# Optimization experiments

Hardware: AMD Instinct MI355X
Metric: run time of the kernel (lower is better)

## Reference

```python
import jax, jax.numpy as jnp
import numpy as np

B, S, D = 4, 4096, 1024
GROUP = 256
HEAD = 128
INNER = 2048


def setup_inputs() -> dict:
    key = jax.random.key(0)
    ks = jax.random.split(key, 16)
    s = 0.02
    return {
        'x': jax.random.normal(ks[0], (B, S, D), jnp.float32),
        'Wv': jax.random.normal(ks[1], (D, INNER), jnp.float32) * s,
        'bv': jnp.zeros((INNER,), jnp.float32),
        'Wg': jax.random.normal(ks[2], (D, INNER), jnp.float32) * s,
        'bg': jnp.zeros((INNER,), jnp.float32),
        'Win': jax.random.normal(ks[3], (D, HEAD), jnp.float32) * s,
        'bin_': jnp.zeros((HEAD,), jnp.float32),
        'Wout': jax.random.normal(ks[4], (INNER, D), jnp.float32) * s,
        'bout': jnp.zeros((D,), jnp.float32),
        'g_qq': 1.0 + jax.random.normal(ks[5], (HEAD,), jnp.float32) * s,
        'b_qq': jnp.zeros((HEAD,), jnp.float32),
        'g_qk': 1.0 + jax.random.normal(ks[6], (HEAD,), jnp.float32) * s,
        'b_qk': jnp.zeros((HEAD,), jnp.float32),
        'g_lq': 1.0 + jax.random.normal(ks[7], (HEAD,), jnp.float32) * s,
        'b_lq': jnp.zeros((HEAD,), jnp.float32),
        'g_lk': 1.0 + jax.random.normal(ks[8], (HEAD,), jnp.float32) * s,
        'b_lk': jnp.zeros((HEAD,), jnp.float32),
    }


def reference(x, Wv, bv, Wg, bg, Win, bin_, Wout, bout,
              g_qq, b_qq, g_qk, b_qk, g_lq, b_lq, g_lk, b_lk):
    b, s, d = x.shape
    g = s // GROUP
    xc = x.reshape(b, g, GROUP, d)                       # [B,G,C,D]
    v = jax.nn.silu(xc @ Wv + bv)                        # [B,G,C,E]
    gate = jax.nn.silu(xc @ Wg + bg)                     # [B,G,C,E]
    x_ = jax.nn.silu(xc @ Win + bin_)                    # [B,G,C,H]
    quad_q = x_ * g_qq + b_qq
    quad_k = x_ * g_qk + b_qk
    lin_q = x_ * g_lq + b_lq
    lin_k = x_ * g_lk + b_lk
    # local quadratic relu^2 attention per chunk
    scale = jnp.asarray(INNER ** 0.5, x.dtype)           # v.size(-1)**0.5
    attn = jnp.einsum('bgns,bgms->bgnm', quad_q, quad_k) / scale
    causal_mask = jnp.triu(jnp.ones((GROUP, GROUP), bool), 1)
    attn = jnp.where(causal_mask, 0.0, attn)
    attn = jnp.square(jax.nn.relu(attn))
    v_quad = jnp.einsum('bgnm,bgme->bgne', attn, v)
    # global causal linear attention: exclusive cumsum of per-chunk k^T v over chunks
    kv = jnp.einsum('bgcs,bgce->bgse', lin_k, v)         # [B,G,H,E]
    kv = jnp.cumsum(kv, axis=1) - kv                     # exclusive over chunk dim
    v_lin = jnp.einsum('bgcs,bgse->bgce', lin_q, kv)
    o = (v_quad + v_lin) * gate
    o = o @ Wout + bout
    return o.reshape(b, s, d)
```

## Files before the change

kernel.cpp:

```cpp
#include <hip/hip_runtime.h>

typedef __attribute__((ext_vector_type(8))) short short8;
typedef __attribute__((ext_vector_type(4))) float floatx4;
typedef __attribute__((ext_vector_type(4))) unsigned short ushort4v;
typedef unsigned short u16;

#define DEV __device__ __forceinline__

DEV u16 f2bf(float f) {
  unsigned int u = __float_as_uint(f);
  u += 0x7fffu + ((u >> 16) & 1u);
  return (u16)(u >> 16);
}
DEV float bf2f(u16 h) { return __uint_as_float(((unsigned int)h) << 16); }
DEV float silu_f(float x) { return x / (1.f + __expf(-x)); }
DEV floatx4 fzero() { floatx4 z = {0.f, 0.f, 0.f, 0.f}; return z; }
DEV floatx4 mfma16(short8 a, short8 b, floatx4 c) {
  return __builtin_amdgcn_mfma_f32_16x16x32_bf16(a, b, c, 0, 0, 0);
}
DEV void gll16(const void* g, void* l) {
  __builtin_amdgcn_global_load_lds((__attribute__((address_space(1))) void*)g,
                                   (__attribute__((address_space(3))) void*)l,
                                   16, 0, 0);
}

__global__ __launch_bounds__(256) void cast_x_kernel(const float* __restrict__ x,
                                                     u16* __restrict__ xb, int n4) {
  int i = blockIdx.x * 256 + threadIdx.x;
  if (i >= n4) return;
  float4 v = ((const float4*)x)[i];
  ushort4v o;
  o[0] = f2bf(v.x); o[1] = f2bf(v.y); o[2] = f2bf(v.z); o[3] = f2bf(v.w);
  *(ushort4v*)&xb[(size_t)i * 4] = o;
}

__global__ __launch_bounds__(256) void transpose_cast_kernel(const float* __restrict__ W,
                                                             u16* __restrict__ WT,
                                                             int K, int N) {
  __shared__ u16 tile[32][36];
  int n0 = blockIdx.x * 32, k0 = blockIdx.y * 32;
  int t = threadIdx.x;
  int r = t >> 3, cs = (t & 7) * 4;
  float4 v = *(const float4*)&W[(size_t)(k0 + r) * N + n0 + cs];
  tile[r][cs + 0] = f2bf(v.x);
  tile[r][cs + 1] = f2bf(v.y);
  tile[r][cs + 2] = f2bf(v.z);
  tile[r][cs + 3] = f2bf(v.w);
  __syncthreads();
  ushort4v o;
  o[0] = tile[cs + 0][r];
  o[1] = tile[cs + 1][r];
  o[2] = tile[cs + 2][r];
  o[3] = tile[cs + 3][r];
  *(ushort4v*)&WT[(size_t)(n0 + r) * K + k0 + cs] = o;
}

DEV void wave_transposed_store(u16* __restrict__ Ct, long chunk_stride,
                               const u16* trw, int chunk, int cbase, int nbase,
                               int lane) {
#pragma unroll
  for (int it = 0; it < 8; ++it) {
    int e_l = it * 8 + (lane >> 3);
    int c_off = (lane & 7) * 8;
    short8 val = *(const short8*)&trw[e_l * 72 + c_off];
    *(short8*)&Ct[(size_t)chunk * chunk_stride + (size_t)(nbase + e_l) * 256 + cbase +
                  c_off] = val;
  }
}

template <int MODE>
__global__ __launch_bounds__(256) void gemm_bt(
    const u16* __restrict__ A, const u16* __restrict__ Bt, int M, int N, int K,
    const float* __restrict__ bias, u16* __restrict__ Cn, float* __restrict__ Cf,
    u16* __restrict__ Ct, long ct_stride, u16* __restrict__ Cn2, u16* __restrict__ Cn3,
    const float* __restrict__ gqq, const float* __restrict__ bqq,
    const float* __restrict__ gqk, const float* __restrict__ bqk,
    const float* __restrict__ glq, const float* __restrict__ blq,
    const float* __restrict__ glk, const float* __restrict__ blk) {
  __shared__ union {
    struct { u16 a[128 * 32]; u16 b[128 * 32]; } st;
    u16 tr[4 * 64 * 72];
  } sm;
  const int t = threadIdx.x;
  const int wave = t >> 6, lane = t & 63;
  const int l15 = lane & 15, l16 = lane >> 4;
  const int n0 = blockIdx.x * 128, m0 = blockIdx.y * 128;
  const int wm = (wave >> 1) * 64, wn = (wave & 1) * 64;

  floatx4 acc[4][4];
#pragma unroll
  for (int i = 0; i < 4; ++i)
#pragma unroll
    for (int j = 0; j < 4; ++j) acc[i][j] = fzero();

  const int c0 = t, c1 = 256 + t;
  const int r0s = c0 >> 2, p0s = c0 & 3;
  const int r1s = c1 >> 2, p1s = c1 & 3;
  const int g0 = p0s ^ ((r0s >> 1) & 3);
  const int g1 = p1s ^ ((r1s >> 1) & 3);
  const u16* pa0 = A + (size_t)(m0 + r0s) * K + g0 * 8;
  const u16* pa1 = A + (size_t)(m0 + r1s) * K + g1 * 8;
  const u16* pb0 = Bt + (size_t)(n0 + r0s) * K + g0 * 8;
  const u16* pb1 = Bt + (size_t)(n0 + r1s) * K + g1 * 8;
  const int sw = (l15 >> 1) & 3;

  for (int k0 = 0; k0 < K; k0 += 32) {
    __syncthreads();
    gll16(pa0 + k0, &sm.st.a[c0 * 8]);
    gll16(pa1 + k0, &sm.st.a[c1 * 8]);
    gll16(pb0 + k0, &sm.st.b[c0 * 8]);
    gll16(pb1 + k0, &sm.st.b[c1 * 8]);
    __syncthreads();
    short8 af[4], bfr[4];
#pragma unroll
    for (int mi = 0; mi < 4; ++mi)
      af[mi] = *(const short8*)&sm.st.a[(wm + mi * 16 + l15) * 32 + (l16 ^ sw) * 8];
#pragma unroll
    for (int ni = 0; ni < 4; ++ni)
      bfr[ni] = *(const short8*)&sm.st.b[(wn + ni * 16 + l15) * 32 + (l16 ^ sw) * 8];
#pragma unroll
    for (int mi = 0; mi < 4; ++mi)
#pragma unroll
      for (int ni = 0; ni < 4; ++ni)
        acc[mi][ni] = mfma16(af[mi], bfr[ni], acc[mi][ni]);
  }
  __syncthreads();

  if constexpr (MODE == 0) {
    u16* trw = &sm.tr[wave * 64 * 72];
#pragma unroll
    for (int mi = 0; mi < 4; ++mi)
#pragma unroll
      for (int ni = 0; ni < 4; ++ni) {
        const int col = n0 + wn + ni * 16 + l15;
        const float bc = bias[col];
#pragma unroll
        for (int r = 0; r < 4; ++r)
          trw[(mi * 16 + l16 * 4 + r) * 72 + ni * 16 + l15] =
              f2bf(silu_f(acc[mi][ni][r] + bc));
      }
#pragma unroll
    for (int it = 0; it < 8; ++it) {
      const int m_l = it * 8 + (lane >> 3);
      const int n_off = (lane & 7) * 8;
      *(short8*)&Cn[(size_t)(m0 + wm + m_l) * N + n0 + wn + n_off] =
          *(const short8*)&trw[m_l * 72 + n_off];
    }
  } else if constexpr (MODE == 3) {
#pragma unroll
    for (int mi = 0; mi < 4; ++mi)
#pragma unroll
      for (int ni = 0; ni < 4; ++ni) {
        const int col = n0 + wn + ni * 16 + l15;
        const float bc = bias[col];
        const int row = m0 + wm + mi * 16 + l16 * 4;
#pragma unroll
        for (int r = 0; r < 4; ++r)
          Cf[(size_t)(row + r) * N + col] = acc[mi][ni][r] + bc;
      }
  } else if constexpr (MODE == 1) {
    u16* trw = &sm.tr[wave * 64 * 72];
#pragma unroll
    for (int mi = 0; mi < 4; ++mi)
#pragma unroll
      for (int ni = 0; ni < 4; ++ni) {
        const int col = n0 + wn + ni * 16 + l15;
        const float bc = bias[col];
        ushort4v p;
#pragma unroll
        for (int r = 0; r < 4; ++r) p[r] = f2bf(silu_f(acc[mi][ni][r] + bc));
        *(ushort4v*)&trw[(ni * 16 + l15) * 72 + mi * 16 + l16 * 4] = p;
      }
    wave_transposed_store(Ct, ct_stride, trw, (m0 + wm) >> 8, (m0 + wm) & 255,
                          n0 + wn, lane);
  } else {
    u16* trw = &sm.tr[wave * 64 * 72];
#pragma unroll
    for (int mi = 0; mi < 4; ++mi)
#pragma unroll
      for (int ni = 0; ni < 4; ++ni) {
        const int col = wn + ni * 16 + l15;
        const float bc = bias[col];
        const float Gqq = gqq[col], Bqq = bqq[col];
        const float Gqk = gqk[col], Bqk = bqk[col];
        const float Glq = glq[col], Blq = blq[col];
        const float Glk = glk[col], Blk = blk[col];
        const int row = m0 + wm + mi * 16 + l16 * 4;
        ushort4v p;
#pragma unroll
        for (int r = 0; r < 4; ++r) {
          const float sv = silu_f(acc[mi][ni][r] + bc);
          const size_t ad = (size_t)(row + r) * N + col;
          Cn[ad] = f2bf(sv * Gqq + Bqq);
          Cn2[ad] = f2bf(sv * Gqk + Bqk);
          Cn3[ad] = f2bf(sv * Glq + Blq);
          p[r] = f2bf(sv * Glk + Blk);
        }
        *(ushort4v*)&trw[(ni * 16 + l15) * 72 + mi * 16 + l16 * 4] = p;
      }
    wave_transposed_store(Ct, ct_stride, trw, (m0 + wm) >> 8, (m0 + wm) & 255, wn,
                          lane);
  }
}

__global__ __launch_bounds__(256) void kv_kernel(const u16* __restrict__ vT,
                                                 const u16* __restrict__ lkT,
                                                 u16* __restrict__ kv) {
  const int chunk = blockIdx.y;
  const int et = blockIdx.x;
  const int w = threadIdx.x >> 6, lane = threadIdx.x & 63;
  const int l15 = lane & 15, l16 = lane >> 4;
  const size_t vb = (size_t)chunk * (2048 * 256) + (size_t)et * (128 * 256);
  const size_t lb = (size_t)chunk * (128 * 256);
  const int we = (w >> 1) * 64, wh = (w & 1) * 64;
  floatx4 acc[4][4];
#pragma unroll
  for (int i = 0; i < 4; ++i)
#pragma unroll
    for (int j = 0; j < 4; ++j) acc[i][j] = fzero();
  for (int kk = 0; kk < 8; ++kk) {
    short8 av[4], bv[4];
#pragma unroll
    for (int mi = 0; mi < 4; ++mi)
      av[mi] = *(const short8*)&vT[vb + (size_t)(we + mi * 16 + l15) * 256 + kk * 32 +
                                   l16 * 8];
#pragma unroll
    for (int ni = 0; ni < 4; ++ni)
      bv[ni] = *(const short8*)&lkT[lb + (size_t)(wh + ni * 16 + l15) * 256 + kk * 32 +
                                    l16 * 8];
#pragma unroll
    for (int mi = 0; mi < 4; ++mi)
#pragma unroll
      for (int ni = 0; ni < 4; ++ni) acc[mi][ni] = mfma16(av[mi], bv[ni], acc[mi][ni]);
  }
  u16* out = kv + (size_t)chunk * (2048 * 128);
#pragma unroll
  for (int mi = 0; mi < 4; ++mi)
#pragma unroll
    for (int ni = 0; ni < 4; ++ni) {
      const int h = wh + ni * 16 + l15;
      const int e = et * 128 + we + mi * 16 + l16 * 4;
#pragma unroll
      for (int r = 0; r < 4; ++r) out[(size_t)(e + r) * 128 + h] = f2bf(acc[mi][ni][r]);
    }
}

__global__ __launch_bounds__(256) void cumsum_kernel(u16* __restrict__ kv) {
  const int idx = blockIdx.x * 256 + threadIdx.x;
  const int b = blockIdx.y;
  float s = 0.f;
  for (int g = 0; g < 16; ++g) {
    const size_t a = (size_t)(b * 16 + g) * 262144 + idx;
    const float v = bf2f(kv[a]);
    kv[a] = f2bf(s);
    s += v;
  }
}

__global__ __launch_bounds__(256) void attn_kernel(
    const u16* __restrict__ qq, const u16* __restrict__ qk, const u16* __restrict__ lq,
    const u16* __restrict__ vT, const u16* __restrict__ kvT,
    u16* __restrict__ gate_op) {
  __shared__ u16 S[64][264];
  const int chunk = blockIdx.y;
  const int e0 = blockIdx.x * 256;
  const int tok0 = chunk * 256;
  const int w = threadIdx.x >> 6, lane = threadIdx.x & 63;
  const int l15 = lane & 15, l16 = lane >> 4;
  const float isc = 0.022097086912079608f;
  const size_t vbase = (size_t)chunk * (2048 * 256);
  const size_t kbase = (size_t)chunk * (2048 * 128);
  const int ew = e0 + w * 64;

  for (int ns = 0; ns < 4; ++ns) {
    const int r0 = ns * 64 + w * 16;
    short8 af[4];
#pragma unroll
    for (int kk = 0; kk < 4; ++kk)
      af[kk] = *(const short8*)&qq[(size_t)(tok0 + r0 + l15) * 128 + kk * 32 + l16 * 8];
    const int mt_cnt = (r0 >> 4) + 1;
    const int mt_all = (ns + 1) * 4;
    const int srow = w * 16 + l16 * 4;
    for (int mt = 0; mt < mt_all; ++mt) {
      if (mt < mt_cnt) {
        floatx4 a = fzero();
#pragma unroll
        for (int kk = 0; kk < 4; ++kk) {
          short8 bq =
              *(const short8*)&qk[(size_t)(tok0 + mt * 16 + l15) * 128 + kk * 32 +
                                  l16 * 8];
          a = mfma16(af[kk], bq, a);
        }
        const int mcol = mt * 16 + l15;
#pragma unroll
        for (int r = 0; r < 4; ++r) {
          const int nrow = r0 + l16 * 4 + r;
          float sv = a[r] * isc;
          sv = (mcol <= nrow) ? sv : 0.f;
          sv = fmaxf(sv, 0.f);
          S[srow + r][mcol] = f2bf(sv * sv);
        }
      } else {
#pragma unroll
        for (int r = 0; r < 4; ++r) S[srow + r][mt * 16 + l15] = (u16)0;
      }
    }
    __syncthreads();

    floatx4 acc[4][4];
#pragma unroll
    for (int i = 0; i < 4; ++i)
#pragma unroll
      for (int j = 0; j < 4; ++j) acc[i][j] = fzero();

    const int ks = (ns + 1) * 2;
    for (int kk = 0; kk < ks; ++kk) {
      short8 sa[4];
#pragma unroll
      for (int nt = 0; nt < 4; ++nt)
        sa[nt] = *(const short8*)&S[nt * 16 + l15][kk * 32 + l16 * 8];
#pragma unroll
      for (int ei = 0; ei < 4; ++ei) {
        short8 vb = *(const short8*)&vT[vbase + (size_t)(ew + ei * 16 + l15) * 256 +
                                        kk * 32 + l16 * 8];
#pragma unroll
        for (int nt = 0; nt < 4; ++nt) acc[nt][ei] = mfma16(sa[nt], vb, acc[nt][ei]);
      }
    }
#pragma unroll
    for (int kk = 0; kk < 4; ++kk) {
      short8 la[4];
#pragma unroll
      for (int nt = 0; nt < 4; ++nt)
        la[nt] = *(const short8*)&lq[(size_t)(tok0 + ns * 64 + nt * 16 + l15) * 128 +
                                     kk * 32 + l16 * 8];
#pragma unroll
      for (int ei = 0; ei < 4; ++ei) {
        short8 kb = *(const short8*)&kvT[kbase + (size_t)(ew + ei * 16 + l15) * 128 +
                                         kk * 32 + l16 * 8];
#pragma unroll
        for (int nt = 0; nt < 4; ++nt) acc[nt][ei] = mfma16(la[nt], kb, acc[nt][ei]);
      }
    }
#pragma unroll
    for (int nt = 0; nt < 4; ++nt)
#pragma unroll
      for (int ei = 0; ei < 4; ++ei) {
        const int e_g = ew + ei * 16 + l15;
        const int nb = tok0 + ns * 64 + nt * 16 + l16 * 4;
#pragma unroll
        for (int r = 0; r < 4; ++r) {
          const size_t ad = (size_t)(nb + r) * 2048 + e_g;
          const float gv = bf2f(gate_op[ad]);
          gate_op[ad] = f2bf(acc[nt][ei][r] * gv);
        }
      }
    __syncthreads();
  }
}

extern "C" void kernel_launch(void* const* d_in, const int* in_sizes, int n_in,
                              void* d_out, int out_size, void* d_ws, size_t ws_size,
                              hipStream_t stream) {
  (void)in_sizes; (void)n_in; (void)out_size; (void)ws_size;
  const float* x = (const float*)d_in[0];
  const float* Wv = (const float*)d_in[1];
  const float* bv = (const float*)d_in[2];
  const float* Wg = (const float*)d_in[3];
  const float* bg = (const float*)d_in[4];
  const float* Win = (const float*)d_in[5];
  const float* bin = (const float*)d_in[6];
  const float* Wout = (const float*)d_in[7];
  const float* bout = (const float*)d_in[8];
  const float* gqq = (const float*)d_in[9];
  const float* bqq = (const float*)d_in[10];
  const float* gqk = (const float*)d_in[11];
  const float* bqk = (const float*)d_in[12];
  const float* glq = (const float*)d_in[13];
  const float* blq = (const float*)d_in[14];
  const float* glk = (const float*)d_in[15];
  const float* blk = (const float*)d_in[16];

  char* p = (char*)d_ws;
  u16* xb = (u16*)p;   p += (size_t)16384 * 1024 * 2;
  u16* wvT = (u16*)p;  p += (size_t)2048 * 1024 * 2;
  u16* wgT = (u16*)p;  p += (size_t)2048 * 1024 * 2;
  u16* winT = (u16*)p; p += (size_t)128 * 1024 * 2;
  u16* woT = (u16*)p;  p += (size_t)1024 * 2048 * 2;
  u16* vTb = (u16*)p;  p += (size_t)64 * 2048 * 256 * 2;
  u16* gate = (u16*)p; p += (size_t)16384 * 2048 * 2;
  u16* qqb = (u16*)p;  p += (size_t)16384 * 128 * 2;
  u16* qkb = (u16*)p;  p += (size_t)16384 * 128 * 2;
  u16* lqb = (u16*)p;  p += (size_t)16384 * 128 * 2;
  u16* lkTb = (u16*)p; p += (size_t)64 * 128 * 256 * 2;
  u16* kvb = (u16*)p;  p += (size_t)64 * 2048 * 128 * 2;

  cast_x_kernel<<<16384, 256, 0, stream>>>(x, xb, 4194304);
  transpose_cast_kernel<<<dim3(64, 32), 256, 0, stream>>>(Wv, wvT, 1024, 2048);
  transpose_cast_kernel<<<dim3(64, 32), 256, 0, stream>>>(Wg, wgT, 1024, 2048);
  transpose_cast_kernel<<<dim3(4, 32), 256, 0, stream>>>(Win, winT, 1024, 128);
  transpose_cast_kernel<<<dim3(32, 64), 256, 0, stream>>>(Wout, woT, 2048, 1024);

  gemm_bt<1><<<dim3(16, 128), 256, 0, stream>>>(
      xb, wvT, 16384, 2048, 1024, bv, nullptr, nullptr, vTb, 2048L * 256, nullptr,
      nullptr, nullptr, nullptr, nullptr, nullptr, nullptr, nullptr, nullptr, nullptr);
  gemm_bt<0><<<dim3(16, 128), 256, 0, stream>>>(
      xb, wgT, 16384, 2048, 1024, bg, gate, nullptr, nullptr, 0, nullptr, nullptr,
      nullptr, nullptr, nullptr, nullptr, nullptr, nullptr, nullptr, nullptr);
  gemm_bt<2><<<dim3(1, 128), 256, 0, stream>>>(
      xb, winT, 16384, 128, 1024, bin, qqb, nullptr, lkTb, 128L * 256, qkb, lqb, gqq,
      bqq, gqk, bqk, glq, blq, glk, blk);

  kv_kernel<<<dim3(16, 64), 256, 0, stream>>>(vTb, lkTb, kvb);
  cumsum_kernel<<<dim3(1024, 4), 256, 0, stream>>>(kvb);
  attn_kernel<<<dim3(8, 64), 256, 0, stream>>>(qqb, qkb, lqb, vTb, kvb, gate);

  gemm_bt<3><<<dim3(8, 128), 256, 0, stream>>>(
      gate, woT, 16384, 1024, 2048, bout, nullptr, (float*)d_out, nullptr, 0, nullptr,
      nullptr, nullptr, nullptr, nullptr, nullptr, nullptr, nullptr, nullptr, nullptr);
}
```

Before: 658.0 us.

## Double GEMM K-tile to 64 and remap blocks per XCD for L2 locality

The GEMM main loop now stages 64-wide K slices instead of 32, with an 8-way XOR swizzle. This halves the number of barrier pairs per tile and doubles the MFMA work between syncs. The grid is flattened to 1D, and block indices are remapped so that each XCD gets a contiguous range of M tiles sweeping all N tiles, which is meant to improve L2 reuse of A rows. The cost is double the LDS staging footprint, which may reduce occupancy.

```diff
diff --git a/kernel.cpp b/kernel.cpp
--- a/kernel.cpp
+++ b/kernel.cpp
@@ -71,58 +71,71 @@
 template <int MODE>
 __global__ __launch_bounds__(256) void gemm_bt(
     const u16* __restrict__ A, const u16* __restrict__ Bt, int M, int N, int K,
-    const float* __restrict__ bias, u16* __restrict__ Cn, float* __restrict__ Cf,
-    u16* __restrict__ Ct, long ct_stride, u16* __restrict__ Cn2, u16* __restrict__ Cn3,
+    int nshift, const float* __restrict__ bias, u16* __restrict__ Cn,
+    float* __restrict__ Cf, u16* __restrict__ Ct, long ct_stride,
+    u16* __restrict__ Cn2, u16* __restrict__ Cn3,
     const float* __restrict__ gqq, const float* __restrict__ bqq,
     const float* __restrict__ gqk, const float* __restrict__ bqk,
     const float* __restrict__ glq, const float* __restrict__ blq,
     const float* __restrict__ glk, const float* __restrict__ blk) {
   __shared__ union {
-    struct { u16 a[128 * 32]; u16 b[128 * 32]; } st;
+    struct { u16 a[128 * 64]; u16 b[128 * 64]; } st;
     u16 tr[4 * 64 * 72];
   } sm;
   const int t = threadIdx.x;
   const int wave = t >> 6, lane = t & 63;
   const int l15 = lane & 15, l16 = lane >> 4;
-  const int n0 = blockIdx.x * 128, m0 = blockIdx.y * 128;
+  const int ell = blockIdx.x;
+  const int xcd = ell & 7, i = ell >> 3;
+  const int mtiles_per_xcd = M >> 10;
+  const int m0 = (xcd * mtiles_per_xcd + (i >> nshift)) * 128;
+  const int n0 = (i & ((1 << nshift) - 1)) * 128;
   const int wm = (wave >> 1) * 64, wn = (wave & 1) * 64;
 
   floatx4 acc[4][4];
 #pragma unroll
-  for (int i = 0; i < 4; ++i)
-#pragma unroll
-    for (int j = 0; j < 4; ++j) acc[i][j] = fzero();
-
-  const int c0 = t, c1 = 256 + t;
-  const int r0s = c0 >> 2, p0s = c0 & 3;
-  const int r1s = c1 >> 2, p1s = c1 & 3;
-  const int g0 = p0s ^ ((r0s >> 1) & 3);
-  const int g1 = p1s ^ ((r1s >> 1) & 3);
-  const u16* pa0 = A + (size_t)(m0 + r0s) * K + g0 * 8;
-  const u16* pa1 = A + (size_t)(m0 + r1s) * K + g1 * 8;
-  const u16* pb0 = Bt + (size_t)(n0 + r0s) * K + g0 * 8;
-  const u16* pb1 = Bt + (size_t)(n0 + r1s) * K + g1 * 8;
-  const int sw = (l15 >> 1) & 3;
-
-  for (int k0 = 0; k0 < K; k0 += 32) {
+  for (int i2 = 0; i2 < 4; ++i2)
+#pragma unroll
+    for (int j = 0; j < 4; ++j) acc[i2][j] = fzero();
+
+  const u16* pa[4];
+  const u16* pb[4];
+#pragma unroll
+  for (int j = 0; j < 4; ++j) {
+    const int c = t + 256 * j;
+    const int r = c >> 3, p = c & 7;
+    const int g = p ^ (r & 7);
+    pa[j] = A + (size_t)(m0 + r) * K + g * 8;
+    pb[j] = Bt + (size_t)(n0 + r) * K + g * 8;
+  }
+
+  for (int k0 = 0; k0 < K; k0 += 64) {
     __syncthreads();
-    gll16(pa0 + k0, &sm.st.a[c0 * 8]);
-    gll16(pa1 + k0, &sm.st.a[c1 * 8]);
-    gll16(pb0 + k0, &sm.st.b[c0 * 8]);
-    gll16(pb1 + k0, &sm.st.b[c1 * 8]);
+#pragma unroll
+    for (int j = 0; j < 4; ++j) {
+      gll16(pa[j] + k0, &sm.st.a[(t + 256 * j) * 8]);
+      gll16(pb[j] + k0, &sm.st.b[(t + 256 * j) * 8]);
+    }
     __syncthreads();
-    short8 af[4], bfr[4];
-#pragma unroll
-    for (int mi = 0; mi < 4; ++mi)
-      af[mi] = *(const short8*)&sm.st.a[(wm + mi * 16 + l15) * 32 + (l16 ^ sw) * 8];
-#pragma unroll
-    for (int ni = 0; ni < 4; ++ni)
-      bfr[ni] = *(const short8*)&sm.st.b[(wn + ni * 16 + l15) * 32 + (l16 ^ sw) * 8];
-#pragma unroll
-    for (int mi = 0; mi < 4; ++mi)
-#pragma unroll
-      for (int ni = 0; ni < 4; ++ni)
-        acc[mi][ni] = mfma16(af[mi], bfr[ni], acc[mi][ni]);
+#pragma unroll
+    for (int s = 0; s < 2; ++s) {
+      short8 af[4], bfr[4];
+#pragma unroll
+      for (int mi = 0; mi < 4; ++mi) {
+        const int wr = wm + mi * 16 + l15;
+        af[mi] = *(const short8*)&sm.st.a[wr * 64 + ((s * 4 + l16) ^ (wr & 7)) * 8];
+      }
+#pragma unroll
+      for (int ni = 0; ni < 4; ++ni) {
+        const int wr = wn + ni * 16 + l15;
+        bfr[ni] = *(const short8*)&sm.st.b[wr * 64 + ((s * 4 + l16) ^ (wr & 7)) * 8];
+      }
+#pragma unroll
+      for (int mi = 0; mi < 4; ++mi)
+#pragma unroll
+        for (int ni = 0; ni < 4; ++ni)
+          acc[mi][ni] = mfma16(af[mi], bfr[ni], acc[mi][ni]);
+    }
   }
   __syncthreads();
 
@@ -401,21 +414,22 @@
   transpose_cast_kernel<<<dim3(4, 32), 256, 0, stream>>>(Win, winT, 1024, 128);
   transpose_cast_kernel<<<dim3(32, 64), 256, 0, stream>>>(Wout, woT, 2048, 1024);
 
-  gemm_bt<1><<<dim3(16, 128), 256, 0, stream>>>(
-      xb, wvT, 16384, 2048, 1024, bv, nullptr, nullptr, vTb, 2048L * 256, nullptr,
+  gemm_bt<1><<<2048, 256, 0, stream>>>(
+      xb, wvT, 16384, 2048, 1024, 4, bv, nullptr, nullptr, vTb, 2048L * 256, nullptr,
       nullptr, nullptr, nullptr, nullptr, nullptr, nullptr, nullptr, nullptr, nullptr);
-  gemm_bt<0><<<dim3(16, 128), 256, 0, stream>>>(
-      xb, wgT, 16384, 2048, 1024, bg, gate, nullptr, nullptr, 0, nullptr, nullptr,
+  gemm_bt<0><<<2048, 256, 0, stream>>>(
+      xb, wgT, 16384, 2048, 1024, 4, bg, gate, nullptr, nullptr, 0, nullptr, nullptr,
       nullptr, nullptr, nullptr, nullptr, nullptr, nullptr, nullptr, nullptr);
-  gemm_bt<2><<<dim3(1, 128), 256, 0, stream>>>(
-      xb, winT, 16384, 128, 1024, bin, qqb, nullptr, lkTb, 128L * 256, qkb, lqb, gqq,
-      bqq, gqk, bqk, glq, blq, glk, blk);
+  gemm_bt<2><<<128, 256, 0, stream>>>(
+      xb, winT, 16384, 128, 1024, 0, bin, qqb, nullptr, lkTb, 128L * 256, qkb, lqb,
+      gqq, bqq, gqk, bqk, glq, blq, glk, blk);
 
   kv_kernel<<<dim3(16, 64), 256, 0, stream>>>(vTb, lkTb, kvb);
   cumsum_kernel<<<dim3(1024, 4), 256, 0, stream>>>(kvb);
   attn_kernel<<<dim3(8, 64), 256, 0, stream>>>(qqb, qkb, lqb, vTb, kvb, gate);
 
-  gemm_bt<3><<<dim3(8, 128), 256, 0, stream>>>(
-      gate, woT, 16384, 1024, 2048, bout, nullptr, (float*)d_out, nullptr, 0, nullptr,
-      nullptr, nullptr, nullptr, nullptr, nullptr, nullptr, nullptr, nullptr, nullptr);
-}
+  gemm_bt<3><<<1024, 256, 0, stream>>>(
+      gate, woT, 16384, 1024, 2048, 3, bout, nullptr, (float*)d_out, nullptr, 0,
+      nullptr, nullptr, nullptr, nullptr, nullptr, nullptr, nullptr, nullptr, nullptr,
+      nullptr);
+}
```

Result: faster. 601.6 us (-8.6%).
